# Performance work log

Measured on AMD Instinct MI355X. Metric: run time of the kernel, lower is better.

## Reference

```python
import jax, jax.numpy as jnp
import numpy as np

NEG_SLOPE = 0.2


def gat_conv(x, src, dst, W, a_src, a_dst, bias, heads, out_ch):
    """PyG-style GATConv (concat=True, self-loops already appended)."""
    N = x.shape[0]
    h = (x @ W).reshape(N, heads, out_ch)            # [N,H,C]
    al_s = jnp.einsum('nhc,hc->nh', h, a_src)        # [N,H]
    al_d = jnp.einsum('nhc,hc->nh', h, a_dst)        # [N,H]
    e = al_s[src] + al_d[dst]                        # [E,H]
    e = jnp.where(e > 0, e, NEG_SLOPE * e)           # leaky_relu
    # segment softmax over edges grouped by destination node
    m = jax.ops.segment_max(e, dst, num_segments=N)  # [N,H]
    ex = jnp.exp(e - m[dst])
    s = jax.ops.segment_sum(ex, dst, num_segments=N)
    alpha = ex / s[dst]                              # [E,H]
    msg = alpha[:, :, None] * h[src]                 # [E,H,C]
    out = jax.ops.segment_sum(msg, dst, num_segments=N)  # [N,H,C]
    return out.reshape(N, heads * out_ch) + bias


def setup_inputs() -> dict:
    key = jax.random.key(0)
    ks = jax.random.split(key, 10)
    N, E = 100000, 1600000
    return {
        'x': jax.random.normal(ks[0], (N, 4), dtype=jnp.float32),
        'edge_index': jax.random.randint(ks[1], (2, E), 0, N, dtype=jnp.int64),
        'W1': jax.random.normal(ks[2], (4, 32), dtype=jnp.float32) * 0.5,
        'a_src1': jax.random.normal(ks[3], (2, 16), dtype=jnp.float32) * 0.5,
        'a_dst1': jax.random.normal(ks[4], (2, 16), dtype=jnp.float32) * 0.5,
        'b1': jax.random.normal(ks[5], (32,), dtype=jnp.float32) * 0.1,
        'W2': jax.random.normal(ks[6], (32, 2), dtype=jnp.float32) * 0.2,
        'a_src2': jax.random.normal(ks[7], (1, 2), dtype=jnp.float32) * 0.5,
        'a_dst2': jax.random.normal(ks[8], (1, 2), dtype=jnp.float32) * 0.5,
        'b2': jax.random.normal(ks[9], (2,), dtype=jnp.float32) * 0.1,
    }


def reference(x, edge_index, W1, a_src1, a_dst1, b1, W2, a_src2, a_dst2, b2):
    N = x.shape[0]
    loop = jnp.arange(N, dtype=edge_index.dtype)     # add_self_loops=True
    src = jnp.concatenate([edge_index[0], loop])
    dst = jnp.concatenate([edge_index[1], loop])
    # dropout(p=0.6) is identity at inference
    h = gat_conv(x, src, dst, W1, a_src1, a_dst1, b1, heads=2, out_ch=16)
    h = jax.nn.elu(h)
    out = gat_conv(h, src, dst, W2, a_src2, a_dst2, b2, heads=1, out_ch=2)
    return out
```

## Files before the change

### kernel.cpp

```cpp
#include <hip/hip_runtime.h>
#include <math.h>

#define NEG_SLOPE 0.2f
#define SCAN_CHUNK 2048
#define ECLAMP 80.0f
#define BUCKET_SHIFT 7
#define BUCKET_MASK 127
#define NPB 128
#define NBMAX 1024
#define EB_CHUNK 2048
#define P4_CAP 3072

__device__ __forceinline__ float lrelu(float e) {
    return e > 0.f ? e : NEG_SLOPE * e;
}

__global__ void k0_prep1(const float* __restrict__ x,
                         const float* __restrict__ W1,
                         const float* __restrict__ a_src1,
                         const float* __restrict__ a_dst1,
                         float* __restrict__ as1,
                         float* __restrict__ ad1,
                         int N) {
    int t = blockIdx.x * blockDim.x + threadIdx.x;
    int n = t >> 5;
    int c = t & 31;
    if (n >= N) return;
    const float4 xv = reinterpret_cast<const float4*>(x)[n];
    float h = xv.x * W1[c] + xv.y * W1[32 + c] + xv.z * W1[64 + c] + xv.w * W1[96 + c];
    float ts = h * a_src1[c];
    float td = h * a_dst1[c];
#pragma unroll
    for (int m = 8; m >= 1; m >>= 1) {
        ts += __shfl_xor(ts, m);
        td += __shfl_xor(td, m);
    }
    if ((c & 15) == 0) {
        int hh = c >> 4;
        as1[n * 2 + hh] = ts;
        ad1[n * 2 + hh] = td;
    }
}

__global__ void p1_hist(const int* __restrict__ dst, int* __restrict__ cmatT,
                        int E, int NB, int nblkE) {
    __shared__ int cnt[NBMAX];
    const int blk = blockIdx.x, tid = threadIdx.x;
    for (int b = tid; b < NB; b += 256) cnt[b] = 0;
    __syncthreads();
    int base = blk * EB_CHUNK;
    int end = min(base + EB_CHUNK, E);
    for (int e = base + tid; e < end; e += 256)
        atomicAdd(&cnt[dst[e] >> BUCKET_SHIFT], 1);
    __syncthreads();
    for (int b = tid; b < NB; b += 256)
        cmatT[(size_t)b * nblkE + blk] = cnt[b];
}

__global__ void k2a_partials(const int* __restrict__ in, int* __restrict__ bsum, int n) {
    __shared__ int ws[4];
    const int tid = threadIdx.x;
    const int lane = tid & 63, wid = tid >> 6;
    int base = blockIdx.x * SCAN_CHUNK + tid * 8;
    int lsum = 0;
#pragma unroll
    for (int i = 0; i < 8; ++i) {
        int idx = base + i;
        lsum += (idx < n) ? in[idx] : 0;
    }
#pragma unroll
    for (int m = 32; m >= 1; m >>= 1) lsum += __shfl_xor(lsum, m);
    if (lane == 0) ws[wid] = lsum;
    __syncthreads();
    if (tid == 0) bsum[blockIdx.x] = ws[0] + ws[1] + ws[2] + ws[3];
}

__global__ void k2b_scanb(const int* __restrict__ bsum, int* __restrict__ bscan, int nb) {
    __shared__ int wsum[16];
    const int tid = threadIdx.x;
    const int lane = tid & 63, wid = tid >> 6;
    int carry = 0;
    for (int base = 0; base < nb; base += 1024) {
        int i = base + tid;
        int v = (i < nb) ? bsum[i] : 0;
        int xx = v;
#pragma unroll
        for (int off = 1; off < 64; off <<= 1) {
            int t = __shfl_up(xx, off);
            if (lane >= off) xx += t;
        }
        if (lane == 63) wsum[wid] = xx;
        __syncthreads();
        int woff = 0;
        for (int w = 0; w < wid; ++w) woff += wsum[w];
        if (i < nb) bscan[i] = carry + woff + xx - v;
        int tot = 0;
        for (int w = 0; w < 16; ++w) tot += wsum[w];
        carry += tot;
        __syncthreads();
    }
}

__global__ void k2c_scan(const int* __restrict__ in, const int* __restrict__ bscan,
                         int* __restrict__ out, int n) {
    __shared__ int ws[4];
    const int tid = threadIdx.x;
    const int lane = tid & 63, wid = tid >> 6;
    int base = blockIdx.x * SCAN_CHUNK + tid * 8;
    int v[8], pre[8];
    int lsum = 0;
#pragma unroll
    for (int i = 0; i < 8; ++i) {
        int idx = base + i;
        v[i] = (idx < n) ? in[idx] : 0;
        pre[i] = lsum;
        lsum += v[i];
    }
    int xs = lsum;
#pragma unroll
    for (int off = 1; off < 64; off <<= 1) {
        int t = __shfl_up(xs, off);
        if (lane >= off) xs += t;
    }
    if (lane == 63) ws[wid] = xs;
    __syncthreads();
    int woff = 0;
    for (int w = 0; w < wid; ++w) woff += ws[w];
    int off0 = bscan[blockIdx.x] + woff + xs - lsum;
#pragma unroll
    for (int i = 0; i < 8; ++i) {
        int idx = base + i;
        if (idx < n) out[idx] = off0 + pre[i];
    }
}

__global__ void p3_scatter(const int* __restrict__ src, const int* __restrict__ dst,
                           const int* __restrict__ cscan, unsigned int* __restrict__ ebuf,
                           int E, int NB, int nblkE) {
    __shared__ int cur[NBMAX];
    const int blk = blockIdx.x, tid = threadIdx.x;
    for (int b = tid; b < NB; b += 256)
        cur[b] = cscan[(size_t)b * nblkE + blk];
    __syncthreads();
    int base = blk * EB_CHUNK;
    int end = min(base + EB_CHUNK, E);
    for (int e = base + tid; e < end; e += 256) {
        int d = dst[e];
        int b = d >> BUCKET_SHIFT;
        int pos = atomicAdd(&cur[b], 1);
        ebuf[pos] = (unsigned int)src[e] | ((unsigned int)(d & BUCKET_MASK) << 24);
    }
}

__global__ void p4_csr(const unsigned int* __restrict__ ebuf,
                       const int* __restrict__ cscan,
                       int* __restrict__ rp, int* __restrict__ esrt,
                       int N, int E, int NB, int nblkE) {
    __shared__ unsigned int ecache[P4_CAP];
    __shared__ int degl[NPB];
    __shared__ int curl[NPB];
    __shared__ int wsum[4];
    const int b = blockIdx.x, tid = threadIdx.x;
    const int lane = tid & 63, wid = tid >> 6;
    int bstart = cscan[(size_t)b * nblkE];
    int bend = (b + 1 < NB) ? cscan[(size_t)(b + 1) * nblkE] : E;
    int cnt = bend - bstart;
    if (tid < NPB) degl[tid] = 0;
    __syncthreads();
    for (int i = tid; i < cnt; i += 256) {
        unsigned int ev = ebuf[bstart + i];
        if (i < P4_CAP) ecache[i] = ev;
        atomicAdd(&degl[ev >> 24], 1);
    }
    __syncthreads();
    int v = (tid < NPB) ? degl[tid] : 0;
    int xs = v;
#pragma unroll
    for (int off = 1; off < 64; off <<= 1) {
        int t = __shfl_up(xs, off);
        if (lane >= off) xs += t;
    }
    if (lane == 63) wsum[wid] = xs;
    __syncthreads();
    int woff = 0;
    for (int w = 0; w < wid; ++w) woff += wsum[w];
    int excl = woff + xs - v;
    int node = (b << BUCKET_SHIFT) + tid;
    if (tid < NPB) {
        if (node < N) rp[node] = bstart + excl;
        curl[tid] = bstart + excl;
    }
    if (b == 0 && tid == 0) rp[N] = E;
    __syncthreads();
    for (int i = tid; i < cnt; i += 256) {
        unsigned int ev = (i < P4_CAP) ? ecache[i] : ebuf[bstart + i];
        int dl = ev >> 24;
        int pos = atomicAdd(&curl[dl], 1);
        esrt[pos] = (int)(ev & 0x00FFFFFFu);
    }
}

__global__ void k4_layer1(const int* __restrict__ rp, const int* __restrict__ esrt,
                          const float* __restrict__ x, const float* __restrict__ as1,
                          const float* __restrict__ ad1, const float* __restrict__ b1,
                          const float* __restrict__ W1,
                          const float* __restrict__ W2, const float* __restrict__ a_src2,
                          const float* __restrict__ a_dst2,
                          float4* __restrict__ h2p, float* __restrict__ ad2,
                          int N) {
    int t = blockIdx.x * blockDim.x + threadIdx.x;
    int n = t >> 3;
    int l = t & 7;
    if (n >= N) return;
    int h = l >> 2;
    int d = l & 3;
    float ad = ad1[n * 2 + h];
    float es = lrelu(as1[n * 2 + h] + ad);
    float ws = __expf(fminf(es, ECLAMP));
    float g0 = ws * x[(size_t)n * 4 + d], g1 = 0.f, g2 = 0.f, g3 = 0.f;
    float s0 = ws, s1 = 0.f, s2 = 0.f, s3 = 0.f;

    int p0 = rp[n], p1 = rp[n + 1];
    int p = p0;
    for (; p + 3 < p1; p += 4) {
        int sa = esrt[p];
        int sb = esrt[p + 1];
        int sc_ = esrt[p + 2];
        int sd = esrt[p + 3];
        float ea = lrelu(as1[(size_t)sa * 2 + h] + ad);
        float eb = lrelu(as1[(size_t)sb * 2 + h] + ad);
        float ec = lrelu(as1[(size_t)sc_ * 2 + h] + ad);
        float ed = lrelu(as1[(size_t)sd * 2 + h] + ad);
        float xa = x[(size_t)sa * 4 + d];
        float xb = x[(size_t)sb * 4 + d];
        float xc = x[(size_t)sc_ * 4 + d];
        float xd = x[(size_t)sd * 4 + d];
        float wa = __expf(fminf(ea, ECLAMP));
        float wb = __expf(fminf(eb, ECLAMP));
        float wc = __expf(fminf(ec, ECLAMP));
        float wd = __expf(fminf(ed, ECLAMP));
        s0 += wa;  g0 += wa * xa;
        s1 += wb;  g1 += wb * xb;
        s2 += wc;  g2 += wc * xc;
        s3 += wd;  g3 += wd * xd;
    }
    for (; p < p1; ++p) {
        int sa = esrt[p];
        float ea = lrelu(as1[(size_t)sa * 2 + h] + ad);
        float xa = x[(size_t)sa * 4 + d];
        float wa = __expf(fminf(ea, ECLAMP));
        s0 += wa;  g0 += wa * xa;
    }
    float s = (s0 + s1) + (s2 + s3);
    float agg = ((g0 + g1) + (g2 + g3)) / s;

    float a2[2][4];
#pragma unroll
    for (int k = 0; k < 8; ++k)
        a2[k >> 2][k & 3] = __shfl(agg, k, 8);

    float t0 = 0.f, t1 = 0.f;
#pragma unroll
    for (int j = 0; j < 4; ++j) {
        int c = l * 4 + j;
        int hc = c >> 4;
        float o = b1[c]
                + a2[hc][0] * W1[c]
                + a2[hc][1] * W1[32 + c]
                + a2[hc][2] * W1[64 + c]
                + a2[hc][3] * W1[96 + c];
        o = o > 0.f ? o : expm1f(o);
        t0 += o * W2[c * 2 + 0];
        t1 += o * W2[c * 2 + 1];
    }
#pragma unroll
    for (int msk = 1; msk <= 4; msk <<= 1) {
        t0 += __shfl_xor(t0, msk);
        t1 += __shfl_xor(t1, msk);
    }
    if (l == 0) {
        float as2v = t0 * a_src2[0] + t1 * a_src2[1];
        float ad2v = t0 * a_dst2[0] + t1 * a_dst2[1];
        h2p[n] = make_float4(t0, t1, as2v, 0.f);
        ad2[n] = ad2v;
    }
}

__global__ void k5_layer2(const int* __restrict__ rp, const int* __restrict__ esrt,
                          const float4* __restrict__ h2p, const float* __restrict__ ad2,
                          const float* __restrict__ b2,
                          float* __restrict__ out, int N) {
    int t = blockIdx.x * blockDim.x + threadIdx.x;
    int n = t >> 3;
    int sub = t & 7;
    if (n >= N) return;
    float ad = ad2[n];
    float s = 0.f, xx = 0.f, yy = 0.f;
    if (sub == 0) {
        float4 hv = h2p[n];
        float w = __expf(fminf(lrelu(hv.z + ad), ECLAMP));
        s = w; xx = w * hv.x; yy = w * hv.y;
    }
    int p0 = rp[n], p1 = rp[n + 1];
    for (int p = p0 + sub; p < p1; p += 8) {
        int sn = esrt[p];
        float4 hv = h2p[sn];
        float w = __expf(fminf(lrelu(hv.z + ad), ECLAMP));
        s += w; xx += w * hv.x; yy += w * hv.y;
    }
#pragma unroll
    for (int msk = 1; msk <= 4; msk <<= 1) {
        s  += __shfl_xor(s, msk);
        xx += __shfl_xor(xx, msk);
        yy += __shfl_xor(yy, msk);
    }
    if (sub == 0) {
        float2 o;
        o.x = xx / s + b2[0];
        o.y = yy / s + b2[1];
        reinterpret_cast<float2*>(out)[n] = o;
    }
}

extern "C" void kernel_launch(void* const* d_in, const int* in_sizes, int n_in,
                              void* d_out, int out_size, void* d_ws, size_t ws_size,
                              hipStream_t stream) {
    const float* x      = (const float*)d_in[0];
    const int*   ei     = (const int*)d_in[1];
    const float* W1     = (const float*)d_in[2];
    const float* a_src1 = (const float*)d_in[3];
    const float* a_dst1 = (const float*)d_in[4];
    const float* b1     = (const float*)d_in[5];
    const float* W2     = (const float*)d_in[6];
    const float* a_src2 = (const float*)d_in[7];
    const float* a_dst2 = (const float*)d_in[8];
    const float* b2     = (const float*)d_in[9];
    float* out = (float*)d_out;

    const int N = in_sizes[0] / 4;
    const int E = in_sizes[1] / 2;
    const int* srcp = ei;
    const int* dstp = ei + E;

    const int NB    = (N + BUCKET_MASK) >> BUCKET_SHIFT;
    const int nblkE = (E + EB_CHUNK - 1) / EB_CHUNK;
    const int M     = NB * nblkE;
    const int nb2   = (M + SCAN_CHUNK - 1) / SCAN_CHUNK;

    char* w = (char*)d_ws;
    float4* h2p  = (float4*)w;  w += (size_t)N * sizeof(float4);
    float*  as1  = (float*)w;   w += (size_t)N * 2 * sizeof(float);
    float*  ad1  = (float*)w;   w += (size_t)N * 2 * sizeof(float);
    float*  ad2  = (float*)w;   w += (size_t)N * sizeof(float);
    int* rp     = (int*)w;      w += (size_t)(N + 4) * sizeof(int);
    int* cmatT  = (int*)w;      w += (size_t)M * sizeof(int);
    int* cscan  = (int*)w;      w += (size_t)M * sizeof(int);
    int* bsum   = (int*)w;      w += (size_t)(nb2 + 4) * sizeof(int);
    int* bscan  = (int*)w;      w += (size_t)(nb2 + 4) * sizeof(int);
    unsigned int* ebuf = (unsigned int*)w;  w += (size_t)E * sizeof(unsigned int);
    int* esrt   = (int*)w;      w += (size_t)E * sizeof(int);

    const int BT = 256;
    k0_prep1<<<((size_t)N * 32 + BT - 1) / BT, BT, 0, stream>>>(
        x, W1, a_src1, a_dst1, as1, ad1, N);
    p1_hist<<<nblkE, 256, 0, stream>>>(dstp, cmatT, E, NB, nblkE);
    k2a_partials<<<nb2, 256, 0, stream>>>(cmatT, bsum, M);
    k2b_scanb<<<1, 1024, 0, stream>>>(bsum, bscan, nb2);
    k2c_scan<<<nb2, 256, 0, stream>>>(cmatT, bscan, cscan, M);
    p3_scatter<<<nblkE, 256, 0, stream>>>(srcp, dstp, cscan, ebuf, E, NB, nblkE);
    p4_csr<<<NB, 256, 0, stream>>>(ebuf, cscan, rp, esrt, N, E, NB, nblkE);
    k4_layer1<<<((size_t)N * 8 + BT - 1) / BT, BT, 0, stream>>>(
        rp, esrt, x, as1, ad1, b1, W1, W2, a_src2, a_dst2, h2p, ad2, N);
    k5_layer2<<<((size_t)N * 8 + BT - 1) / BT, BT, 0, stream>>>(
        rp, esrt, h2p, ad2, b2, out, N);
}
```

Baseline: 182.8 us.

## Keep CSR bucket edges in registers and split layer-1 gather across edges

```diff
diff --git a/kernel.cpp b/kernel.cpp
--- a/kernel.cpp
+++ b/kernel.cpp
@@ -9,7 +9,7 @@
 #define NPB 128
 #define NBMAX 1024
 #define EB_CHUNK 2048
-#define P4_CAP 3072
+#define P4_MAXIT 16
 
 __device__ __forceinline__ float lrelu(float e) {
     return e > 0.f ? e : NEG_SLOPE * e;
@@ -156,8 +156,8 @@
                        const int* __restrict__ cscan,
                        int* __restrict__ rp, int* __restrict__ esrt,
                        int N, int E, int NB, int nblkE) {
-    __shared__ unsigned int ecache[P4_CAP];
     __shared__ int degl[NPB];
+    __shared__ int base_[NPB];
     __shared__ int curl[NPB];
     __shared__ int wsum[4];
     const int b = blockIdx.x, tid = threadIdx.x;
@@ -167,11 +167,19 @@
     int cnt = bend - bstart;
     if (tid < NPB) degl[tid] = 0;
     __syncthreads();
-    for (int i = tid; i < cnt; i += 256) {
-        unsigned int ev = ebuf[bstart + i];
-        if (i < P4_CAP) ecache[i] = ev;
-        atomicAdd(&degl[ev >> 24], 1);
-    }
+    unsigned int evs[P4_MAXIT];
+    int rks[P4_MAXIT];
+#pragma unroll
+    for (int it = 0; it < P4_MAXIT; ++it) {
+        int i = it * 256 + tid;
+        if (i < cnt) {
+            unsigned int ev = ebuf[bstart + i];
+            evs[it] = ev;
+            rks[it] = atomicAdd(&degl[ev >> 24], 1);
+        }
+    }
+    for (int i = P4_MAXIT * 256 + tid; i < cnt; i += 256)
+        atomicAdd(&degl[ebuf[bstart + i] >> 24], 1);
     __syncthreads();
     int v = (tid < NPB) ? degl[tid] : 0;
     int xs = v;
@@ -188,15 +196,27 @@
     int node = (b << BUCKET_SHIFT) + tid;
     if (tid < NPB) {
         if (node < N) rp[node] = bstart + excl;
-        curl[tid] = bstart + excl;
+        base_[tid] = bstart + excl;
     }
     if (b == 0 && tid == 0) rp[N] = E;
     __syncthreads();
-    for (int i = tid; i < cnt; i += 256) {
-        unsigned int ev = (i < P4_CAP) ? ecache[i] : ebuf[bstart + i];
-        int dl = ev >> 24;
-        int pos = atomicAdd(&curl[dl], 1);
-        esrt[pos] = (int)(ev & 0x00FFFFFFu);
+    if (cnt <= P4_MAXIT * 256) {
+#pragma unroll
+        for (int it = 0; it < P4_MAXIT; ++it) {
+            int i = it * 256 + tid;
+            if (i < cnt) {
+                unsigned int ev = evs[it];
+                esrt[base_[ev >> 24] + rks[it]] = (int)(ev & 0x00FFFFFFu);
+            }
+        }
+    } else {
+        if (tid < NPB) curl[tid] = base_[tid];
+        __syncthreads();
+        for (int i = tid; i < cnt; i += 256) {
+            unsigned int ev = ebuf[bstart + i];
+            int pos = atomicAdd(&curl[ev >> 24], 1);
+            esrt[pos] = (int)(ev & 0x00FFFFFFu);
+        }
     }
 }
 
@@ -210,65 +230,55 @@
                           int N) {
     int t = blockIdx.x * blockDim.x + threadIdx.x;
     int n = t >> 3;
-    int l = t & 7;
+    int j = t & 7;
     if (n >= N) return;
-    int h = l >> 2;
-    int d = l & 3;
-    float ad = ad1[n * 2 + h];
-    float es = lrelu(as1[n * 2 + h] + ad);
-    float ws = __expf(fminf(es, ECLAMP));
-    float g0 = ws * x[(size_t)n * 4 + d], g1 = 0.f, g2 = 0.f, g3 = 0.f;
-    float s0 = ws, s1 = 0.f, s2 = 0.f, s3 = 0.f;
-
+    const float2* as1v = reinterpret_cast<const float2*>(as1);
+    const float2* ad1v = reinterpret_cast<const float2*>(ad1);
+    const float4* x4 = reinterpret_cast<const float4*>(x);
+    float2 adv = ad1v[n];
+    float s0 = 0.f, s1 = 0.f;
+    float g00 = 0.f, g01 = 0.f, g02 = 0.f, g03 = 0.f;
+    float g10 = 0.f, g11 = 0.f, g12 = 0.f, g13 = 0.f;
+    if (j == 0) {
+        float2 av = as1v[n];
+        float4 xv = x4[n];
+        float w0 = __expf(fminf(lrelu(av.x + adv.x), ECLAMP));
+        float w1 = __expf(fminf(lrelu(av.y + adv.y), ECLAMP));
+        s0 = w0; s1 = w1;
+        g00 = w0 * xv.x; g01 = w0 * xv.y; g02 = w0 * xv.z; g03 = w0 * xv.w;
+        g10 = w1 * xv.x; g11 = w1 * xv.y; g12 = w1 * xv.z; g13 = w1 * xv.w;
+    }
     int p0 = rp[n], p1 = rp[n + 1];
-    int p = p0;
-    for (; p + 3 < p1; p += 4) {
-        int sa = esrt[p];
-        int sb = esrt[p + 1];
-        int sc_ = esrt[p + 2];
-        int sd = esrt[p + 3];
-        float ea = lrelu(as1[(size_t)sa * 2 + h] + ad);
-        float eb = lrelu(as1[(size_t)sb * 2 + h] + ad);
-        float ec = lrelu(as1[(size_t)sc_ * 2 + h] + ad);
-        float ed = lrelu(as1[(size_t)sd * 2 + h] + ad);
-        float xa = x[(size_t)sa * 4 + d];
-        float xb = x[(size_t)sb * 4 + d];
-        float xc = x[(size_t)sc_ * 4 + d];
-        float xd = x[(size_t)sd * 4 + d];
-        float wa = __expf(fminf(ea, ECLAMP));
-        float wb = __expf(fminf(eb, ECLAMP));
-        float wc = __expf(fminf(ec, ECLAMP));
-        float wd = __expf(fminf(ed, ECLAMP));
-        s0 += wa;  g0 += wa * xa;
-        s1 += wb;  g1 += wb * xb;
-        s2 += wc;  g2 += wc * xc;
-        s3 += wd;  g3 += wd * xd;
-    }
-    for (; p < p1; ++p) {
-        int sa = esrt[p];
-        float ea = lrelu(as1[(size_t)sa * 2 + h] + ad);
-        float xa = x[(size_t)sa * 4 + d];
-        float wa = __expf(fminf(ea, ECLAMP));
-        s0 += wa;  g0 += wa * xa;
-    }
-    float s = (s0 + s1) + (s2 + s3);
-    float agg = ((g0 + g1) + (g2 + g3)) / s;
-
-    float a2[2][4];
-#pragma unroll
-    for (int k = 0; k < 8; ++k)
-        a2[k >> 2][k & 3] = __shfl(agg, k, 8);
-
+    for (int p = p0 + j; p < p1; p += 8) {
+        int sn = esrt[p];
+        float2 av = as1v[sn];
+        float4 xv = x4[sn];
+        float w0 = __expf(fminf(lrelu(av.x + adv.x), ECLAMP));
+        float w1 = __expf(fminf(lrelu(av.y + adv.y), ECLAMP));
+        s0 += w0; s1 += w1;
+        g00 += w0 * xv.x; g01 += w0 * xv.y; g02 += w0 * xv.z; g03 += w0 * xv.w;
+        g10 += w1 * xv.x; g11 += w1 * xv.y; g12 += w1 * xv.z; g13 += w1 * xv.w;
+    }
+#pragma unroll
+    for (int msk = 1; msk <= 4; msk <<= 1) {
+        s0 += __shfl_xor(s0, msk);   s1 += __shfl_xor(s1, msk);
+        g00 += __shfl_xor(g00, msk); g01 += __shfl_xor(g01, msk);
+        g02 += __shfl_xor(g02, msk); g03 += __shfl_xor(g03, msk);
+        g10 += __shfl_xor(g10, msk); g11 += __shfl_xor(g11, msk);
+        g12 += __shfl_xor(g12, msk); g13 += __shfl_xor(g13, msk);
+    }
+    float r0 = 1.f / s0, r1 = 1.f / s1;
+    bool h1sel = (j >= 4);
+    float ax = h1sel ? g10 * r1 : g00 * r0;
+    float ay = h1sel ? g11 * r1 : g01 * r0;
+    float az = h1sel ? g12 * r1 : g02 * r0;
+    float aw = h1sel ? g13 * r1 : g03 * r0;
     float t0 = 0.f, t1 = 0.f;
 #pragma unroll
-    for (int j = 0; j < 4; ++j) {
-        int c = l * 4 + j;
-        int hc = c >> 4;
-        float o = b1[c]
-                + a2[hc][0] * W1[c]
-                + a2[hc][1] * W1[32 + c]
-                + a2[hc][2] * W1[64 + c]
-                + a2[hc][3] * W1[96 + c];
+    for (int jj = 0; jj < 4; ++jj) {
+        int c = j * 4 + jj;
+        float o = b1[c] + ax * W1[c] + ay * W1[32 + c]
+                + az * W1[64 + c] + aw * W1[96 + c];
         o = o > 0.f ? o : expm1f(o);
         t0 += o * W2[c * 2 + 0];
         t1 += o * W2[c * 2 + 1];
@@ -278,7 +288,7 @@
         t0 += __shfl_xor(t0, msk);
         t1 += __shfl_xor(t1, msk);
     }
-    if (l == 0) {
+    if (j == 0) {
         float as2v = t0 * a_src2[0] + t1 * a_src2[1];
         float ad2v = t0 * a_dst2[0] + t1 * a_dst2[1];
         h2p[n] = make_float4(t0, t1, as2v, 0.f);
```

After: 182.6 us. No clear change (-0.1%).
